# Optimization experiments

Hardware: AMD Instinct MI355X
Metric: run time of the kernel (lower is better)

The kernel has to match this reference:

```python
import jax, jax.numpy as jnp
import numpy as np

B, S, D, H = 2, 2048, 1024, 16
HD = D // H  # head_dim = 64


def setup_inputs() -> dict:
    key = jax.random.key(0)
    ks = jax.random.split(key, 5)
    scale = 0.02
    x = jax.random.normal(ks[0], (B, S, D), dtype=jnp.float32)
    W_q = jax.random.normal(ks[1], (D, D), dtype=jnp.float32) * scale
    W_k = jax.random.normal(ks[2], (D, D), dtype=jnp.float32) * scale
    W_v = jax.random.normal(ks[3], (D, D), dtype=jnp.float32) * scale
    W_o = jax.random.normal(ks[4], (D, D), dtype=jnp.float32) * scale
    z = jnp.zeros((D,), dtype=jnp.float32)
    return {"x": x, "W_q": W_q, "b_q": z, "W_k": W_k, "b_k": z,
            "W_v": W_v, "b_v": z, "W_o": W_o, "b_o": z}


def _proj_heads(x, W, b):
    # [B,S,D] @ [D,D] -> [B,S,D] -> [B,H,S,HD]
    y = x @ W + b
    return y.reshape(x.shape[0], x.shape[1], H, HD).transpose(0, 2, 1, 3)


def reference(x, W_q, b_q, W_k, b_k, W_v, b_v, W_o, b_o):
    b, s, d = x.shape
    q = _proj_heads(x, W_q, b_q)  # [B,H,S,HD]
    k = _proj_heads(x, W_k, b_k)
    v = _proj_heads(x, W_v, b_v)
    scale = 1.0 / jnp.sqrt(jnp.float32(HD))
    # [B,H,S,S] causal scores
    scores = jnp.einsum('bhqe,bhke->bhqk', q, k) * scale
    causal = jnp.tril(jnp.ones((s, s), dtype=bool))
    scores = jnp.where(causal[None, None], scores, jnp.finfo(scores.dtype).min)
    attn = jax.nn.softmax(scores, axis=-1)
    ctx = jnp.einsum('bhqk,bhke->bhqe', attn, v)  # [B,H,S,HD]
    ctx = ctx.transpose(0, 2, 1, 3).reshape(b, s, d)
    return ctx @ W_o + b_o
```

## Files before the change

### kernel.cpp

```cpp
#include <hip/hip_runtime.h>
#include <hip/hip_bf16.h>
#include <math.h>


#define Bdim  2
#define Sdim  2048
#define Ddim  1024
#define Hn    16
#define HDdim 64
#define Mdim  (Bdim * Sdim)

#define QSCALE 0.18033688011112042f

typedef unsigned short ushort_t;
typedef __attribute__((ext_vector_type(8))) short bfrag;
typedef __attribute__((ext_vector_type(4))) float f4;

__device__ __forceinline__ ushort_t f2bf(float f) {
    union { float f; unsigned int i; } c;
    c.f = f;
    unsigned int x = c.i;
    unsigned int r = (x + 0x7fffu + ((x >> 16) & 1u)) >> 16;
    return (ushort_t)r;
}

__device__ __forceinline__ void glds16(const void* g, void* l) {
    __builtin_amdgcn_global_load_lds(
        (const __attribute__((address_space(1))) unsigned int*)g,
        (__attribute__((address_space(3))) unsigned int*)l, 16, 0, 0);
}

__global__ __launch_bounds__(256)
void prep(const float* __restrict__ x, ushort_t* __restrict__ xb,
          const float* __restrict__ W0, const float* __restrict__ W1,
          const float* __restrict__ W2, const float* __restrict__ W3,
          ushort_t* __restrict__ qkvT, ushort_t* __restrict__ oT)
{
    __shared__ ushort_t t[64][72];
    const int tid = threadIdx.x;
    const int z = blockIdx.z;

    if (z >= 4) {
        size_t blk = (size_t)(z - 4) * 256 + blockIdx.y * 16 + blockIdx.x;
        size_t i = (blk * 256 + tid) * 8;
        float4 a = *(const float4*)(x + i);
        float4 b = *(const float4*)(x + i + 4);
        ushort_t o[8] = {f2bf(a.x), f2bf(a.y), f2bf(a.z), f2bf(a.w),
                         f2bf(b.x), f2bf(b.y), f2bf(b.z), f2bf(b.w)};
        *(bfrag*)(xb + i) = *(const bfrag*)o;
        return;
    }

    const float* W = (z == 0) ? W0 : (z == 1) ? W1 : (z == 2) ? W2 : W3;
    const int k0 = blockIdx.y * 64, n0 = blockIdx.x * 64;

    const int r = tid >> 4, c4 = (tid & 15) * 4;
    #pragma unroll
    for (int rr = 0; rr < 4; ++rr) {
        int k = r + rr * 16;
        float4 v = *(const float4*)&W[(size_t)(k0 + k) * Ddim + n0 + c4];
        t[c4 + 0][k] = f2bf(v.x);
        t[c4 + 1][k] = f2bf(v.y);
        t[c4 + 2][k] = f2bf(v.z);
        t[c4 + 3][k] = f2bf(v.w);
    }
    __syncthreads();
    ushort_t* out = (z < 3) ? (qkvT + (size_t)z * Ddim * Ddim) : oT;
    const int n = tid >> 2, kc = (tid & 3) * 16;
    *(bfrag*)&out[(size_t)(n0 + n) * Ddim + k0 + kc] = *(const bfrag*)&t[n][kc];
    *(bfrag*)&out[(size_t)(n0 + n) * Ddim + k0 + kc + 8] = *(const bfrag*)&t[n][kc + 8];
}

template <int MODE>
__global__ __launch_bounds__(256)
void gemm_mfma(const ushort_t* __restrict__ A, const ushort_t* __restrict__ Bt,
               const float* __restrict__ bQ, const float* __restrict__ bK,
               const float* __restrict__ bV,
               ushort_t* __restrict__ oQ, ushort_t* __restrict__ oK,
               ushort_t* __restrict__ oVt, float* __restrict__ oF)
{
    __shared__ ushort_t As[2][128 * 32];
    __shared__ ushort_t Bs[2][128 * 32];

    const int tid  = threadIdx.x;
    const int lane = tid & 63;
    const int w    = tid >> 6;
    const int l15  = lane & 15;
    const int quad = lane >> 4;
    const int wr   = w >> 1, wc = w & 1;
    const int m0 = blockIdx.y * 128;
    const int n0 = blockIdx.x * 128;

    f4 acc[4][4];
    #pragma unroll
    for (int i = 0; i < 4; ++i)
        #pragma unroll
        for (int j = 0; j < 4; ++j) acc[i][j] = (f4){0.f, 0.f, 0.f, 0.f};

    const int srow  = w * 32 + (lane >> 2);
    const int selem = (lane & 3) * 8;
    const ushort_t* gA = A  + (size_t)(m0 + srow) * Ddim + selem;
    const ushort_t* gB = Bt + (size_t)(n0 + srow) * Ddim + selem;
    char* lA0 = (char*)As + (w * 32) * 64;
    char* lB0 = (char*)Bs + (w * 32) * 64;

    glds16(gA,             lA0);
    glds16(gA + 16 * Ddim, lA0 + 1024);
    glds16(gB,             lB0);
    glds16(gB + 16 * Ddim, lB0 + 1024);
    __syncthreads();

    int buf = 0;
    for (int kk = 0; kk < Ddim; kk += 32) {
        if (kk + 32 < Ddim) {
            const int nb = buf ^ 1;
            glds16(gA + kk + 32,            lA0 + nb * 8192);
            glds16(gA + 16 * Ddim + kk + 32, lA0 + nb * 8192 + 1024);
            glds16(gB + kk + 32,            lB0 + nb * 8192);
            glds16(gB + 16 * Ddim + kk + 32, lB0 + nb * 8192 + 1024);
        }

        bfrag Af[4], Bf[4];
        #pragma unroll
        for (int i = 0; i < 4; ++i)
            Af[i] = *(const bfrag*)&As[buf][(wr * 64 + i * 16 + l15) * 32 + quad * 8];
        #pragma unroll
        for (int j = 0; j < 4; ++j)
            Bf[j] = *(const bfrag*)&Bs[buf][(wc * 64 + j * 16 + l15) * 32 + quad * 8];
        #pragma unroll
        for (int i = 0; i < 4; ++i)
            #pragma unroll
            for (int j = 0; j < 4; ++j)
                acc[i][j] = __builtin_amdgcn_mfma_f32_16x16x32_bf16(Af[i], Bf[j], acc[i][j], 0, 0, 0);

        __syncthreads();
        buf ^= 1;
    }

    if constexpr (MODE == 0) {
        const int sel   = n0 >> 10;
        const int dbase = n0 & 1023;
        const float* bias = (sel == 0) ? bQ : (sel == 1) ? bK : bV;
        ushort_t* dst = (sel == 0) ? oQ : (sel == 1) ? oK : oVt;
        #pragma unroll
        for (int j = 0; j < 4; ++j) {
            int dn = dbase + wc * 64 + j * 16 + l15;
            float bv = bias[dn];
            int h = dn >> 6, e = dn & 63;
            #pragma unroll
            for (int i = 0; i < 4; ++i) {
                #pragma unroll
                for (int r = 0; r < 4; ++r) {
                    int m = m0 + wr * 64 + i * 16 + quad * 4 + r;
                    int b = m >> 11, s = m & 2047;
                    float v = acc[i][j][r] + bv;
                    if (sel == 0) v *= QSCALE;
                    if (sel < 2)
                        dst[((((size_t)b * Hn + h) * Sdim + s) << 6) + e] = f2bf(v);
                    else
                        dst[(((size_t)b * Hn + h) * HDdim + e) * Sdim + s] = f2bf(v);
                }
            }
        }
    } else {
        #pragma unroll
        for (int j = 0; j < 4; ++j) {
            int n = n0 + wc * 64 + j * 16 + l15;
            float bv = bQ[n];
            #pragma unroll
            for (int i = 0; i < 4; ++i)
                #pragma unroll
                for (int r = 0; r < 4; ++r) {
                    int m = m0 + wr * 64 + i * 16 + quad * 4 + r;
                    oF[(size_t)m * Ddim + n] = acc[i][j][r] + bv;
                }
        }
    }
}

#define NBH (Bdim * Hn)

#define MFMA16(a, b, c) __builtin_amdgcn_mfma_f32_16x16x32_bf16(a, b, c, 0, 0, 0)
#define EXP2(x) __builtin_amdgcn_exp2f(x)

__global__ __launch_bounds__(256, 4)
void flash_mfma(const ushort_t* __restrict__ Q, const ushort_t* __restrict__ K,
                const ushort_t* __restrict__ Vt, ushort_t* __restrict__ ctx)
{
    __shared__ ushort_t KtS[2][64 * 64];
    __shared__ ushort_t VsS[2][64 * 64];
    __shared__ ushort_t PTS[4][1024];

    const int tid  = threadIdx.x;
    const int lane = tid & 63;
    const int w    = tid >> 6;
    const int l15  = lane & 15;
    const int quad = lane >> 4;

    const int qb = 31 - (blockIdx.x >> 5);
    const int bh = blockIdx.x & 31;
    const int q0 = qb * 64;
    const int qw = q0 + w * 16;
    const int ntiles = qb + 1;

    const ushort_t* Qrow = Q + ((size_t)bh * Sdim + qw + l15) * HDdim;
    const bfrag Qf0 = *(const bfrag*)(Qrow + quad * 8);
    const bfrag Qf1 = *(const bfrag*)(Qrow + 32 + quad * 8);

    const ushort_t* Kp = K  + (size_t)bh * Sdim * HDdim;
    const ushort_t* Vp = Vt + (size_t)bh * HDdim * Sdim;

    const int srow = w * 8 + (lane >> 3);
    const int scol = ((lane & 7) ^ (lane >> 3)) * 8;
    const ushort_t* gK = Kp + (size_t)srow * HDdim + scol;
    const ushort_t* gV = Vp + (size_t)srow * Sdim + scol;
    char* ldsK = (char*)KtS + w * 1024;
    char* ldsV = (char*)VsS + w * 1024;
    ushort_t* PTw = PTS[w];

    const int sw = l15 & 7;
    const int c0 = (quad ^ sw) << 4;
    const int c1 = c0 ^ 64;
    const char* KtR = (const char*)KtS + l15 * 128;
    const char* VsR = (const char*)VsS + l15 * 128;

    f4 O[4];
    #pragma unroll
    for (int c = 0; c < 4; ++c) O[c] = (f4){0.f, 0.f, 0.f, 0.f};
    float m_prev = -INFINITY, l_run = 0.f;

    glds16(gK,                       ldsK);
    glds16(gK + 32 * HDdim,          ldsK + 4096);
    glds16(gV,                       ldsV);
    glds16(gV + (size_t)32 * Sdim,   ldsV + 4096);
    __syncthreads();

    for (int kt = 0; kt < ntiles - 1; ++kt) {
        const int k0  = kt << 6;
        const int buf = kt & 1;
        const int nb  = buf ^ 1;

        {
            const size_t kn = (size_t)(k0 + 64);
            glds16(gK + kn * HDdim,               ldsK + nb * 8192);
            glds16(gK + (kn + 32) * HDdim,        ldsK + nb * 8192 + 4096);
            glds16(gV + kn,                       ldsV + nb * 8192);
            glds16(gV + kn + (size_t)32 * Sdim,   ldsV + nb * 8192 + 4096);
        }

        const char* Kb = KtR + buf * 8192;
        const char* Vb = VsR + buf * 8192;

        float p[4][4];
        #pragma unroll
        for (int h = 0; h < 4; ++h) {
            bfrag a0 = *(const bfrag*)(Kb + h * 2048 + c0);
            bfrag a1 = *(const bfrag*)(Kb + h * 2048 + c1);
            f4 s = (f4){0.f, 0.f, 0.f, 0.f};
            s = MFMA16(a0, Qf0, s);
            s = MFMA16(a1, Qf1, s);
            #pragma unroll
            for (int r = 0; r < 4; ++r) p[h][r] = s[r];
        }

        float mh0 = fmaxf(fmaxf(p[0][0], p[0][1]), fmaxf(p[0][2], p[0][3]));
        float mh1 = fmaxf(fmaxf(p[1][0], p[1][1]), fmaxf(p[1][2], p[1][3]));
        float mh2 = fmaxf(fmaxf(p[2][0], p[2][1]), fmaxf(p[2][2], p[2][3]));
        float mh3 = fmaxf(fmaxf(p[3][0], p[3][1]), fmaxf(p[3][2], p[3][3]));
        float mt = fmaxf(fmaxf(mh0, mh1), fmaxf(mh2, mh3));
        mt = fmaxf(mt, __shfl_xor(mt, 16, 64));
        mt = fmaxf(mt, __shfl_xor(mt, 32, 64));

        if (__any(mt > m_prev + 8.f)) {
            float m_new = fmaxf(m_prev, mt);
            float alpha = EXP2(m_prev - m_new);
            l_run *= alpha;
            #pragma unroll
            for (int r = 0; r < 4; ++r) {
                float ar = __shfl(alpha, (lane & 48) + quad * 4 + r, 64);
                #pragma unroll
                for (int c = 0; c < 4; ++c) O[c][r] *= ar;
            }
            m_prev = m_new;
        }

        float rs0 = 0.f, rs1 = 0.f, rs2 = 0.f, rs3 = 0.f;
        #pragma unroll
        for (int r = 0; r < 4; ++r) {
            p[0][r] = EXP2(p[0][r] - m_prev); rs0 += p[0][r];
            p[1][r] = EXP2(p[1][r] - m_prev); rs1 += p[1][r];
            p[2][r] = EXP2(p[2][r] - m_prev); rs2 += p[2][r];
            p[3][r] = EXP2(p[3][r] - m_prev); rs3 += p[3][r];
        }
        float rsum = (rs0 + rs1) + (rs2 + rs3);
        rsum += __shfl_xor(rsum, 16, 64);
        rsum += __shfl_xor(rsum, 32, 64);
        l_run += rsum;

        #pragma unroll
        for (int h = 0; h < 4; ++h) {
            ushort_t pk[4] = {f2bf(p[h][0]), f2bf(p[h][1]),
                              f2bf(p[h][2]), f2bf(p[h][3])};
            *(uint2*)&PTw[((((h << 1) + (quad >> 1)) * 16 + l15) << 3) + (quad & 1) * 4] =
                *(const uint2*)pk;
        }
        bfrag pA0 = *(const bfrag*)&PTw[lane * 8];
        bfrag pA1 = *(const bfrag*)&PTw[512 + lane * 8];

        #pragma unroll
        for (int c = 0; c < 4; ++c) {
            bfrag v0 = *(const bfrag*)(Vb + c * 2048 + c0);
            bfrag v1 = *(const bfrag*)(Vb + c * 2048 + c1);
            O[c] = MFMA16(pA0, v0, O[c]);
            O[c] = MFMA16(pA1, v1, O[c]);
        }

        __syncthreads();
    }

    {
        const int buf = (ntiles - 1) & 1;
        const char* Kb = KtR + buf * 8192;
        const char* Vb = VsR + buf * 8192;

        float p[4][4];
        float mt = -INFINITY;
        #pragma unroll
        for (int h = 0; h < 4; ++h) {
            if (h <= w) {
                bfrag a0 = *(const bfrag*)(Kb + h * 2048 + c0);
                bfrag a1 = *(const bfrag*)(Kb + h * 2048 + c1);
                f4 s = (f4){0.f, 0.f, 0.f, 0.f};
                s = MFMA16(a0, Qf0, s);
                s = MFMA16(a1, Qf1, s);
                if (h == w) {
                    #pragma unroll
                    for (int r = 0; r < 4; ++r) {
                        float v = (quad * 4 + r <= l15) ? s[r] : -INFINITY;
                        p[h][r] = v;
                        mt = fmaxf(mt, v);
                    }
                } else {
                    #pragma unroll
                    for (int r = 0; r < 4; ++r) {
                        p[h][r] = s[r];
                        mt = fmaxf(mt, s[r]);
                    }
                }
            } else {
                #pragma unroll
                for (int r = 0; r < 4; ++r) p[h][r] = -INFINITY;
            }
        }
        mt = fmaxf(mt, __shfl_xor(mt, 16, 64));
        mt = fmaxf(mt, __shfl_xor(mt, 32, 64));

        if (__any(mt > m_prev + 8.f)) {
            float m_new = fmaxf(m_prev, mt);
            float alpha = EXP2(m_prev - m_new);
            l_run *= alpha;
            #pragma unroll
            for (int r = 0; r < 4; ++r) {
                float ar = __shfl(alpha, (lane & 48) + quad * 4 + r, 64);
                #pragma unroll
                for (int c = 0; c < 4; ++c) O[c][r] *= ar;
            }
            m_prev = m_new;
        }

        float rsum = 0.f;
        #pragma unroll
        for (int h = 0; h < 4; ++h)
            #pragma unroll
            for (int r = 0; r < 4; ++r) {
                float e = EXP2(p[h][r] - m_prev);
                p[h][r] = e;
                rsum += e;
            }
        rsum += __shfl_xor(rsum, 16, 64);
        rsum += __shfl_xor(rsum, 32, 64);
        l_run += rsum;

        #pragma unroll
        for (int h = 0; h < 4; ++h) {
            ushort_t pk[4] = {f2bf(p[h][0]), f2bf(p[h][1]),
                              f2bf(p[h][2]), f2bf(p[h][3])};
            *(uint2*)&PTw[((((h << 1) + (quad >> 1)) * 16 + l15) << 3) + (quad & 1) * 4] =
                *(const uint2*)pk;
        }
        bfrag pA0 = *(const bfrag*)&PTw[lane * 8];
        #pragma unroll
        for (int c = 0; c < 4; ++c) {
            bfrag v0 = *(const bfrag*)(Vb + c * 2048 + c0);
            O[c] = MFMA16(pA0, v0, O[c]);
        }
        if (w >= 2) {
            bfrag pA1 = *(const bfrag*)&PTw[512 + lane * 8];
            #pragma unroll
            for (int c = 0; c < 4; ++c) {
                bfrag v1 = *(const bfrag*)(Vb + c * 2048 + c1);
                O[c] = MFMA16(pA1, v1, O[c]);
            }
        }
    }

    const int b = bh >> 4, h = bh & 15;
    #pragma unroll
    for (int r = 0; r < 4; ++r) {
        float inv_l = 1.0f / __shfl(l_run, (lane & 48) + quad * 4 + r, 64);
        size_t base = ((size_t)b * Sdim + qw + quad * 4 + r) * Ddim + h * HDdim + l15;
        #pragma unroll
        for (int c = 0; c < 4; ++c)
            ctx[base + c * 16] = f2bf(O[c][r] * inv_l);
    }
}

extern "C" void kernel_launch(void* const* d_in, const int* in_sizes, int n_in,
                              void* d_out, int out_size, void* d_ws, size_t ws_size,
                              hipStream_t stream)
{
    const int NX = Mdim * Ddim;
    const int NW = Ddim * Ddim;
    int xi = 0, wi[4] = {1, 3, 5, 7}, bi[4] = {2, 4, 6, 8}, nw = 0, nb = 0;
    bool sized = true;
    for (int i = 0; i < 9; ++i) {
        if (in_sizes[i] == NX) xi = i;
        else if (in_sizes[i] == NW) { if (nw < 4) wi[nw++] = i; }
        else if (in_sizes[i] == Ddim) { if (nb < 4) bi[nb++] = i; }
        else sized = false;
    }
    int iWq, iWk, iWv, iWo, ibq, ibk, ibv, ibo;
    if (!sized || xi == 0) {
        xi = 0; iWq = 1; ibq = 2; iWk = 3; ibk = 4; iWv = 5; ibv = 6; iWo = 7; ibo = 8;
    } else {
        iWk = wi[0]; iWo = wi[1]; iWq = wi[2]; iWv = wi[3];
        ibk = bi[0]; ibo = bi[1]; ibq = bi[2]; ibv = bi[3];
    }

    const float* x  = (const float*)d_in[xi];
    const float* Wq = (const float*)d_in[iWq];
    const float* bq = (const float*)d_in[ibq];
    const float* Wk = (const float*)d_in[iWk];
    const float* bk = (const float*)d_in[ibk];
    const float* Wv = (const float*)d_in[iWv];
    const float* bv = (const float*)d_in[ibv];
    const float* Wo = (const float*)d_in[iWo];
    const float* bo = (const float*)d_in[ibo];
    float* out = (float*)d_out;

    const size_t elems = (size_t)Mdim * Ddim;
    const size_t welems = (size_t)Ddim * Ddim;
    ushort_t* Qb    = (ushort_t*)d_ws;
    ushort_t* Kb    = Qb + elems;
    ushort_t* Vtb   = Kb + elems;
    ushort_t* Cb    = Vtb + elems;
    ushort_t* xb    = Cb + elems;
    ushort_t* qkvT  = xb + elems;
    ushort_t* WoT   = qkvT + 3 * welems;

    dim3 blk(256);
    prep<<<dim3(16, 16, 12), blk, 0, stream>>>(x, xb, Wq, Wk, Wv, Wo, qkvT, WoT);

    gemm_mfma<0><<<dim3(3 * Ddim / 128, Mdim / 128), blk, 0, stream>>>(
        xb, qkvT, bq, bk, bv, Qb, Kb, Vtb, nullptr);

    flash_mfma<<<dim3(32 * NBH), blk, 0, stream>>>(Qb, Kb, Vtb, Cb);

    gemm_mfma<1><<<dim3(Ddim / 128, Mdim / 128), blk, 0, stream>>>(
        Cb, WoT, bo, nullptr, nullptr, nullptr, nullptr, nullptr, out);
}
```

Before: 192.5 us.

## Triple-buffer GEMM LDS tiles with explicit vmcnt waits and single barrier

Changes the projection GEMM's shared-memory staging from double to triple buffering. It prefetches two k-tiles ahead and uses s_waitcnt vmcnt plus one raw barrier per iteration in place of two __syncthreads. The aim is to hide more global-load latency and cut per-step synchronization. In exchange it uses 50% more LDS, which may reduce occupancy, and its correctness depends on the hand-placed waitcnt counts.

```diff
diff --git a/kernel.cpp b/kernel.cpp
--- a/kernel.cpp
+++ b/kernel.cpp
@@ -79,8 +79,8 @@
                ushort_t* __restrict__ oQ, ushort_t* __restrict__ oK,
                ushort_t* __restrict__ oVt, float* __restrict__ oF)
 {
-    __shared__ ushort_t As[2][128 * 32];
-    __shared__ ushort_t Bs[2][128 * 32];
+    __shared__ ushort_t As[3][128 * 32];
+    __shared__ ushort_t Bs[3][128 * 32];
 
     const int tid  = threadIdx.x;
     const int lane = tid & 63;
@@ -104,37 +104,47 @@
     char* lA0 = (char*)As + (w * 32) * 64;
     char* lB0 = (char*)Bs + (w * 32) * 64;
 
-    glds16(gA,             lA0);
-    glds16(gA + 16 * Ddim, lA0 + 1024);
-    glds16(gB,             lB0);
-    glds16(gB + 16 * Ddim, lB0 + 1024);
-    __syncthreads();
-
-    int buf = 0;
-    for (int kk = 0; kk < Ddim; kk += 32) {
-        if (kk + 32 < Ddim) {
-            const int nb = buf ^ 1;
-            glds16(gA + kk + 32,            lA0 + nb * 8192);
-            glds16(gA + 16 * Ddim + kk + 32, lA0 + nb * 8192 + 1024);
-            glds16(gB + kk + 32,            lB0 + nb * 8192);
-            glds16(gB + 16 * Ddim + kk + 32, lB0 + nb * 8192 + 1024);
+    const int NT = Ddim / 32;
+
+    glds16(gA,                  lA0);
+    glds16(gA + 16 * Ddim,      lA0 + 1024);
+    glds16(gB,                  lB0);
+    glds16(gB + 16 * Ddim,      lB0 + 1024);
+    glds16(gA + 32,             lA0 + 8192);
+    glds16(gA + 16 * Ddim + 32, lA0 + 8192 + 1024);
+    glds16(gB + 32,             lB0 + 8192);
+    glds16(gB + 16 * Ddim + 32, lB0 + 8192 + 1024);
+
+    int bc = 0;
+    for (int t = 0; t < NT; ++t) {
+        if (t < NT - 1) asm volatile("s_waitcnt vmcnt(4)" ::: "memory");
+        else            asm volatile("s_waitcnt vmcnt(0)" ::: "memory");
+        __builtin_amdgcn_s_barrier();
+        asm volatile("" ::: "memory");
+
+        if (t + 2 < NT) {
+            int b2 = bc + 2; if (b2 >= 3) b2 -= 3;
+            const int kk = (t + 2) * 32;
+            glds16(gA + kk,             lA0 + b2 * 8192);
+            glds16(gA + 16 * Ddim + kk, lA0 + b2 * 8192 + 1024);
+            glds16(gB + kk,             lB0 + b2 * 8192);
+            glds16(gB + 16 * Ddim + kk, lB0 + b2 * 8192 + 1024);
         }
 
         bfrag Af[4], Bf[4];
         #pragma unroll
         for (int i = 0; i < 4; ++i)
-            Af[i] = *(const bfrag*)&As[buf][(wr * 64 + i * 16 + l15) * 32 + quad * 8];
+            Af[i] = *(const bfrag*)&As[bc][(wr * 64 + i * 16 + l15) * 32 + quad * 8];
         #pragma unroll
         for (int j = 0; j < 4; ++j)
-            Bf[j] = *(const bfrag*)&Bs[buf][(wc * 64 + j * 16 + l15) * 32 + quad * 8];
+            Bf[j] = *(const bfrag*)&Bs[bc][(wc * 64 + j * 16 + l15) * 32 + quad * 8];
         #pragma unroll
         for (int i = 0; i < 4; ++i)
             #pragma unroll
             for (int j = 0; j < 4; ++j)
                 acc[i][j] = __builtin_amdgcn_mfma_f32_16x16x32_bf16(Af[i], Bf[j], acc[i][j], 0, 0, 0);
 
-        __syncthreads();
-        buf ^= 1;
+        bc += 1; if (bc >= 3) bc -= 3;
     }
 
     if constexpr (MODE == 0) {
```

Result: slower. 202.8 us (+5.4%).
